# Kernel optimization log

Measured on AMD Instinct MI355X. Metric: run time of the kernel, lower is better.

Reference implementation:

```python
import jax, jax.numpy as jnp
import numpy as np

EMBED = 1024
HEADS = 16
HEAD_DIM = EMBED // HEADS


def setup_inputs() -> dict:
    key = jax.random.key(0)
    ks = jax.random.split(key, 8)
    N, L = 4, 2048
    inp = {
        "values": jax.random.normal(ks[0], (N, L, EMBED), dtype=jnp.float32),
        "keys": jax.random.normal(ks[1], (N, L, EMBED), dtype=jnp.float32),
        "query": jax.random.normal(ks[2], (N, L, EMBED), dtype=jnp.float32),
        # per-head-dim projections (torch Linear: y = x @ W.T), no bias
        "Wv": jax.random.normal(ks[3], (HEAD_DIM, HEAD_DIM), dtype=jnp.float32) * (1.0 / np.sqrt(HEAD_DIM)),
        "Wk": jax.random.normal(ks[4], (HEAD_DIM, HEAD_DIM), dtype=jnp.float32) * (1.0 / np.sqrt(HEAD_DIM)),
        "Wq": jax.random.normal(ks[5], (HEAD_DIM, HEAD_DIM), dtype=jnp.float32) * (1.0 / np.sqrt(HEAD_DIM)),
        # output projection with bias
        "Wo": jax.random.normal(ks[6], (EMBED, EMBED), dtype=jnp.float32) * (1.0 / np.sqrt(EMBED)),
        "bo": jax.random.normal(ks[7], (EMBED,), dtype=jnp.float32) * 0.01,
    }
    return inp


def reference(values, keys, query, Wv, Wk, Wq, Wo, bo):
    N, Lq, _ = query.shape
    Lv = values.shape[1]
    Lk = keys.shape[1]
    # split heads: [N, L, H, D]
    v = values.reshape(N, Lv, HEADS, HEAD_DIM)
    k = keys.reshape(N, Lk, HEADS, HEAD_DIM)
    q = query.reshape(N, Lq, HEADS, HEAD_DIM)
    # per-head-dim linear projections (x @ W.T)
    v = jnp.einsum("nlhd,ed->nlhe", v, Wv)
    k = jnp.einsum("nlhd,ed->nlhe", k, Wk)
    q = jnp.einsum("nlhd,ed->nlhe", q, Wq)
    # scores: [N, H, Q, K]; note scale is sqrt(embed_size), matching source
    energy = jnp.einsum("nqhd,nkhd->nhqk", q, k)
    attention = jax.nn.softmax(energy / jnp.sqrt(jnp.float32(EMBED)), axis=-1)
    # weighted values: [N, Q, H, D] -> [N, Q, E]
    out = jnp.einsum("nhql,nlhd->nqhd", attention, v).reshape(N, Lq, EMBED)
    # output projection
    return out @ Wo.T + bo
```

## Files before the change

### kernel.cpp

```cpp
#include <hip/hip_runtime.h>
#include <hip/hip_bf16.h>

typedef __bf16 bf16;
typedef __bf16 bf16x2 __attribute__((ext_vector_type(2)));
typedef __bf16 bf16x4 __attribute__((ext_vector_type(4)));
typedef __bf16 bf16x8 __attribute__((ext_vector_type(8)));
typedef float f32x4 __attribute__((ext_vector_type(4)));

#define MFMA16(a, b, c) __builtin_amdgcn_mfma_f32_16x16x32_bf16((a), (b), (c), 0, 0, 0)

#if __has_builtin(__builtin_amdgcn_exp2f)
#define EXP2(x) __builtin_amdgcn_exp2f(x)
#else
#define EXP2(x) exp2f(x)
#endif

constexpr int EMBED = 1024;
constexpr int HEADS = 16;
constexpr int HD = 64;
constexpr int SEQ = 2048;
constexpr int LDSP = 72;
constexpr int SXTP = 76;
constexpr int WO_N = EMBED * EMBED;

#define QSCALE 0.04508422082f

static __device__ __forceinline__ unsigned pack2(float a, float b) {
    bf16x2 t;
    t[0] = (bf16)a;
    t[1] = (bf16)b;
    return __builtin_bit_cast(unsigned, t);
}
#define SWAP32(x, y) asm("v_permlane32_swap_b32 %0, %1" : "+v"(x), "+v"(y))
#define SWAP16(x, y) asm("v_permlane16_swap_b32 %0, %1" : "+v"(x), "+v"(y))

__global__ __launch_bounds__(256) void convert_weights(
    const float* __restrict__ Wo, const float* __restrict__ Wq,
    const float* __restrict__ Wk, const float* __restrict__ Wv,
    bf16* __restrict__ Wob, bf16* __restrict__ Wqb,
    bf16* __restrict__ Wkb, bf16* __restrict__ Wvb) {
    int gid = blockIdx.x * 256 + threadIdx.x;
    int base = gid * 8;
    const float* src;
    bf16* dst;
    float sc = 1.0f;
    int off;
    if (base < WO_N) {
        src = Wo; dst = Wob; off = base;
    } else {
        int j = base - WO_N;
        int w = j >> 12;
        off = j & 4095;
        src = (w == 0) ? Wq : (w == 1) ? Wk : Wv;
        dst = (w == 0) ? Wqb : (w == 1) ? Wkb : Wvb;
        if (w == 0) sc = QSCALE;
    }
    float4 a = *(const float4*)(src + off);
    float4 b = *(const float4*)(src + off + 4);
    bf16x8 o;
    o[0] = (bf16)(a.x * sc); o[1] = (bf16)(a.y * sc);
    o[2] = (bf16)(a.z * sc); o[3] = (bf16)(a.w * sc);
    o[4] = (bf16)(b.x * sc); o[5] = (bf16)(b.y * sc);
    o[6] = (bf16)(b.z * sc); o[7] = (bf16)(b.w * sc);
    *(bf16x8*)(dst + off) = o;
}

__global__ __launch_bounds__(256) void proj_kernel(
    const float* __restrict__ Vx, const float* __restrict__ Kx, const float* __restrict__ Qx,
    const bf16* __restrict__ Wqb, const bf16* __restrict__ Wkb, const bf16* __restrict__ Wvb,
    bf16* __restrict__ Vt, bf16* __restrict__ Kp, bf16* __restrict__ Qp) {
    __shared__ __align__(16) bf16 sT[64 * LDSP];
    __shared__ __align__(16) bf16 sXT[64 * SXTP];
    int t = threadIdx.x, lane = t & 63, wq = t >> 6;
    int m = lane & 15, q8 = lane >> 4;
    int rowbase = blockIdx.x * 64;
    int Arow = rowbase + wq * 16 + m;
    const float* Xs[3] = {Qx, Kx, Vx};
    const bf16* Ws[3] = {Wqb, Wkb, Wvb};
    f32x4 z = {0.f, 0.f, 0.f, 0.f};

    for (int ts = 0; ts < 3; ts++) {
        bf16x8 af[2];
        for (int c = 0; c < 2; c++) {
            const float* s = Xs[ts] + (size_t)Arow * 64 + c * 32 + q8 * 8;
            float4 x0 = *(const float4*)s;
            float4 x1 = *(const float4*)(s + 4);
            bf16x8 a;
            a[0] = (bf16)x0.x; a[1] = (bf16)x0.y; a[2] = (bf16)x0.z; a[3] = (bf16)x0.w;
            a[4] = (bf16)x1.x; a[5] = (bf16)x1.y; a[6] = (bf16)x1.z; a[7] = (bf16)x1.w;
            af[c] = a;
        }
        bf16x8 bfr[4][2];
        for (int nt = 0; nt < 4; nt++)
            for (int c = 0; c < 2; c++)
                bfr[nt][c] = *(const bf16x8*)(Ws[ts] + (nt * 16 + m) * 64 + c * 32 + q8 * 8);
        f32x4 acc[4] = {z, z, z, z};
        for (int c = 0; c < 2; c++)
            for (int nt = 0; nt < 4; nt++)
                acc[nt] = MFMA16(af[c], bfr[nt][c], acc[nt]);

        if (ts < 2) {
            __syncthreads();
            for (int nt = 0; nt < 4; nt++)
                for (int jr = 0; jr < 4; jr++)
                    sT[(wq * 16 + q8 * 4 + jr) * LDSP + nt * 16 + m] = (bf16)acc[nt][jr];
            __syncthreads();
            int r = t >> 2, c4 = t & 3;
            int R = rowbase + r;
            int h = R & 15, l = (R >> 4) & 2047, n = R >> 15;
            bf16* dst = ((ts == 0) ? Qp : Kp) + ((size_t)(n * HEADS + h) * SEQ + l) * HD + c4 * 16;
            bf16x8 v0 = *(const bf16x8*)&sT[r * LDSP + c4 * 16];
            bf16x8 v1 = *(const bf16x8*)&sT[r * LDSP + c4 * 16 + 8];
            *(bf16x8*)dst = v0;
            *(bf16x8*)(dst + 8) = v1;
        } else {
            for (int nt = 0; nt < 4; nt++) {
                bf16x4 pv;
                pv[0] = (bf16)acc[nt][0]; pv[1] = (bf16)acc[nt][1];
                pv[2] = (bf16)acc[nt][2]; pv[3] = (bf16)acc[nt][3];
                *(bf16x4*)&sXT[(nt * 16 + m) * SXTP + wq * 16 + q8 * 4] = pv;
            }
            __syncthreads();
            int n = rowbase >> 15, l0 = (rowbase >> 4) & 2047;
            for (int i = t; i < 1024; i += 256) {
                int e = i & 63, hh = i >> 6;
                bf16x4 pv;
                pv[0] = sXT[e * SXTP + 0 * 16 + hh];
                pv[1] = sXT[e * SXTP + 1 * 16 + hh];
                pv[2] = sXT[e * SXTP + 2 * 16 + hh];
                pv[3] = sXT[e * SXTP + 3 * 16 + hh];
                *(bf16x4*)(Vt + ((size_t)(n * HEADS + hh) * HD + e) * SEQ + l0) = pv;
            }
        }
    }
}

__global__ __launch_bounds__(256, 2) void flash_kernel(
    const bf16* __restrict__ Qp, const bf16* __restrict__ Kp, const bf16* __restrict__ Vt,
    bf16* __restrict__ O) {
    int nh = blockIdx.x, qt = blockIdx.y;
    int n = nh >> 4, h = nh & 15;
    int t = threadIdx.x, lane = t & 63, wq = t >> 6;
    int m = lane & 15, q8 = lane >> 4;
    __shared__ __align__(16) bf16 sK[64 * LDSP];
    __shared__ __align__(16) bf16 sV[64 * LDSP];
    size_t nhs = (size_t)nh;
    int qb = qt * 256 + wq * 64;
    const bf16* Qb = Qp + (nhs * SEQ + qb) * HD;
    const bf16* Kb = Kp + nhs * SEQ * HD;
    const bf16* Vb = Vt + nhs * (size_t)HD * SEQ;

    bool isK = t < 128;
    int t2 = isK ? t : t - 128;
    int srow = t2 >> 1, shalf = t2 & 1;
    const bf16* sbase = isK ? (Kb + (size_t)srow * HD + shalf * 32)
                            : (Vb + (size_t)srow * SEQ + shalf * 32);
    size_t sstride = isK ? (size_t)HD : 1;
    bf16* ldst = (isK ? sK : sV) + srow * LDSP + shalf * 32;

    bf16x8 qf[4][2];
    for (int ntq = 0; ntq < 4; ntq++)
        for (int c = 0; c < 2; c++)
            qf[ntq][c] = *(const bf16x8*)(Qb + (ntq * 16 + m) * HD + c * 32 + q8 * 8);

    bf16x8 ones;
    for (int i = 0; i < 8; i++) ones[i] = (bf16)1.0f;

    f32x4 z = {0.f, 0.f, 0.f, 0.f};
    f32x4 accO[4][4];
    for (int a = 0; a < 4; a++)
        for (int b = 0; b < 4; b++) accO[a][b] = z;
    f32x4 accL[4] = {z, z, z, z};

    bf16x8 stg[4];
    auto load_stage = [&](int kb) {
#pragma unroll
        for (int j = 0; j < 4; j++)
            stg[j] = *(const bf16x8*)(sbase + (size_t)kb * sstride + j * 8);
    };
    auto write_stage = [&]() {
#pragma unroll
        for (int j = 0; j < 4; j++)
            *(bf16x8*)(ldst + j * 8) = stg[j];
    };

    load_stage(0);
    write_stage();
    __syncthreads();
    load_stage(64);

    for (int kb = 0; kb < SEQ; kb += 64) {
        bf16x8 kf[4][2];
#pragma unroll
        for (int kt = 0; kt < 4; kt++)
#pragma unroll
            for (int c = 0; c < 2; c++)
                kf[kt][c] = *(const bf16x8*)&sK[(kt * 16 + m) * LDSP + c * 32 + q8 * 8];
        bf16x8 vf[4][2];
#pragma unroll
        for (int dt = 0; dt < 4; dt++)
#pragma unroll
            for (int c = 0; c < 2; c++)
                vf[dt][c] = *(const bf16x8*)&sV[(dt * 16 + m) * LDSP + c * 32 + q8 * 8];
        __syncthreads();
        write_stage();
        __syncthreads();
        load_stage((kb + 128) & (SEQ - 1));

#pragma unroll
        for (int ntq = 0; ntq < 4; ntq++) {
            f32x4 st[4];
#pragma unroll
            for (int kt = 0; kt < 4; kt++) st[kt] = z;
#pragma unroll
            for (int c = 0; c < 2; c++)
#pragma unroll
                for (int kt = 0; kt < 4; kt++)
                    st[kt] = MFMA16(kf[kt][c], qf[ntq][c], st[kt]);
            f32x4 pr[4];
#pragma unroll
            for (int kt = 0; kt < 4; kt++) {
                pr[kt][0] = EXP2(st[kt][0]);
                pr[kt][1] = EXP2(st[kt][1]);
                pr[kt][2] = EXP2(st[kt][2]);
                pr[kt][3] = EXP2(st[kt][3]);
            }
            bf16x8 pf[2];
#pragma unroll
            for (int c = 0; c < 2; c++) {
                unsigned dw[4];
#pragma unroll
                for (int i = 0; i < 2; i++) {
                    unsigned u = pack2(pr[2 * c][2 * i], pr[2 * c][2 * i + 1]);
                    unsigned v = pack2(pr[2 * c + 1][2 * i], pr[2 * c + 1][2 * i + 1]);
                    SWAP32(u, v);
                    SWAP16(u, v);
                    dw[i] = u;
                    dw[2 + i] = v;
                }
                union { unsigned u[4]; bf16x8 v; } cvt;
                cvt.u[0] = dw[0]; cvt.u[1] = dw[1];
                cvt.u[2] = dw[2]; cvt.u[3] = dw[3];
                pf[c] = cvt.v;
            }
#pragma unroll
            for (int c = 0; c < 2; c++) {
#pragma unroll
                for (int dt = 0; dt < 4; dt++)
                    accO[ntq][dt] = MFMA16(pf[c], vf[dt][c], accO[ntq][dt]);
                accL[ntq] = MFMA16(pf[c], ones, accL[ntq]);
            }
        }
    }

    for (int mtq = 0; mtq < 4; mtq++)
        for (int j = 0; j < 4; j++) {
            float iv = 1.0f / accL[mtq][j];
            int q = qb + mtq * 16 + q8 * 4 + j;
            size_t ro = ((size_t)n * SEQ + q) * EMBED + h * HD;
            for (int dt = 0; dt < 4; dt++)
                O[ro + dt * 16 + m] = (bf16)(accO[mtq][dt][j] * iv);
        }
}

__global__ __launch_bounds__(256) void outproj_kernel(
    const bf16* __restrict__ O, const bf16* __restrict__ Wob,
    const float* __restrict__ bo, float* __restrict__ out) {
    int et = blockIdx.x, qt = blockIdx.y;
    int t = threadIdx.x, lane = t & 63, wq = t >> 6;
    int m = lane & 15, q8 = lane >> 4;
    int qb = qt * 128 + wq * 32;
    const bf16* Ob = O + (size_t)qb * EMBED;
    const bf16* Wb = Wob + (size_t)et * 64 * EMBED;
    f32x4 z = {0.f, 0.f, 0.f, 0.f};
    f32x4 acc[2][4];
    for (int a = 0; a < 2; a++)
        for (int b = 0; b < 4; b++) acc[a][b] = z;

    bf16x8 afA[2], bfA[4], afB[2], bfB[4];
    auto loadA = [&](int kk) {
        for (int mt = 0; mt < 2; mt++)
            afA[mt] = *(const bf16x8*)(Ob + (size_t)(mt * 16 + m) * EMBED + kk + q8 * 8);
        for (int nt = 0; nt < 4; nt++)
            bfA[nt] = *(const bf16x8*)(Wb + (size_t)(nt * 16 + m) * EMBED + kk + q8 * 8);
    };
    auto loadB = [&](int kk) {
        for (int mt = 0; mt < 2; mt++)
            afB[mt] = *(const bf16x8*)(Ob + (size_t)(mt * 16 + m) * EMBED + kk + q8 * 8);
        for (int nt = 0; nt < 4; nt++)
            bfB[nt] = *(const bf16x8*)(Wb + (size_t)(nt * 16 + m) * EMBED + kk + q8 * 8);
    };
    loadA(0);
    loadB(32);
    for (int kk = 0; kk < EMBED; kk += 64) {
        for (int mt = 0; mt < 2; mt++)
            for (int nt = 0; nt < 4; nt++)
                acc[mt][nt] = MFMA16(afA[mt], bfA[nt], acc[mt][nt]);
        loadA((kk + 64) & (EMBED - 1));
        for (int mt = 0; mt < 2; mt++)
            for (int nt = 0; nt < 4; nt++)
                acc[mt][nt] = MFMA16(afB[mt], bfB[nt], acc[mt][nt]);
        loadB((kk + 96) & (EMBED - 1));
    }
    for (int nt = 0; nt < 4; nt++) {
        int col = et * 64 + nt * 16 + m;
        float bias = bo[col];
        for (int mt = 0; mt < 2; mt++)
            for (int j = 0; j < 4; j++) {
                int q = qb + mt * 16 + q8 * 4 + j;
                out[(size_t)q * EMBED + col] = acc[mt][nt][j] + bias;
            }
    }
}

extern "C" void kernel_launch(void* const* d_in, const int* in_sizes, int n_in,
                              void* d_out, int out_size, void* d_ws, size_t ws_size,
                              hipStream_t stream) {
    const float* values = (const float*)d_in[0];
    const float* keys   = (const float*)d_in[1];
    const float* query  = (const float*)d_in[2];
    const float* Wv     = (const float*)d_in[3];
    const float* Wk     = (const float*)d_in[4];
    const float* Wq     = (const float*)d_in[5];
    const float* Wo     = (const float*)d_in[6];
    const float* bo     = (const float*)d_in[7];
    float* out = (float*)d_out;

    char* ws = (char*)d_ws;
    bf16* Qp  = (bf16*)(ws);
    bf16* Kp  = (bf16*)(ws + (size_t)(16 << 20));
    bf16* Vt  = (bf16*)(ws + (size_t)(32 << 20));
    bf16* O   = (bf16*)(ws + (size_t)(48 << 20));
    bf16* Wob = (bf16*)(ws + (size_t)(64 << 20));
    bf16* Wqb = (bf16*)(ws + (size_t)(66 << 20));
    bf16* Wkb = (bf16*)(ws + (size_t)(66 << 20) + 8192);
    bf16* Wvb = (bf16*)(ws + (size_t)(66 << 20) + 16384);

    hipLaunchKernelGGL(convert_weights, dim3(518), dim3(256), 0, stream,
                       Wo, Wq, Wk, Wv, Wob, Wqb, Wkb, Wvb);
    hipLaunchKernelGGL(proj_kernel, dim3(2048), dim3(256), 0, stream,
                       values, keys, query, Wqb, Wkb, Wvb, Vt, Kp, Qp);
    hipLaunchKernelGGL(flash_kernel, dim3(64, 8), dim3(256), 0, stream, Qp, Kp, Vt, O);
    hipLaunchKernelGGL(outproj_kernel, dim3(16, 64), dim3(256), 0, stream, O, Wob, bo, out);
}
```

Measured before the change: 334.7 us.

## Tile output projection GEMM through LDS with 128x128 blocks and XCD-aware mapping

Rewrites the output projection so each block stages 128x128 tiles of O and Wo in LDS with register-prefetched double buffering. Each wave then computes a 64x64 sub-tile, replacing the old scheme where every wave read its operands directly from global memory. The grid becomes 1D with an XCD-aware remap so neighbouring query tiles share an L2, and launch bounds now request 2 blocks per CU. The intent is to cut redundant global traffic and raise MFMA reuse per load, at the cost of more LDS, extra barriers and higher register pressure.

```diff
diff --git a/kernel.cpp b/kernel.cpp
--- a/kernel.cpp
+++ b/kernel.cpp
@@ -263,51 +263,79 @@
         }
 }
 
-__global__ __launch_bounds__(256) void outproj_kernel(
+__global__ __launch_bounds__(256, 2) void outproj_kernel(
     const bf16* __restrict__ O, const bf16* __restrict__ Wob,
     const float* __restrict__ bo, float* __restrict__ out) {
-    int et = blockIdx.x, qt = blockIdx.y;
+    __shared__ __align__(16) bf16 sA[128 * LDSP];
+    __shared__ __align__(16) bf16 sB[128 * LDSP];
+    int bid = blockIdx.x;
+    int xcd = bid & 7, idx = bid >> 3;
+    int qt = xcd * 8 + (idx & 7), et = idx >> 3;
     int t = threadIdx.x, lane = t & 63, wq = t >> 6;
     int m = lane & 15, q8 = lane >> 4;
-    int qb = qt * 128 + wq * 32;
-    const bf16* Ob = O + (size_t)qb * EMBED;
-    const bf16* Wb = Wob + (size_t)et * 64 * EMBED;
+    int wr = wq >> 1, wc = wq & 1;
+    int qb = qt * 128, cb = et * 128;
+
+    bool isA = t < 128;
+    int r = t & 127;
+    const bf16* sbase = isA ? (O + (size_t)(qb + r) * EMBED)
+                            : (Wob + (size_t)(cb + r) * EMBED);
+    bf16* ldst = (isA ? sA : sB) + r * LDSP;
+
+    bf16x8 stg[8];
+    auto load_stage = [&](int kk) {
+#pragma unroll
+        for (int j = 0; j < 8; j++)
+            stg[j] = *(const bf16x8*)(sbase + kk + j * 8);
+    };
+    auto write_stage = [&]() {
+#pragma unroll
+        for (int j = 0; j < 8; j++)
+            *(bf16x8*)(ldst + j * 8) = stg[j];
+    };
+
     f32x4 z = {0.f, 0.f, 0.f, 0.f};
-    f32x4 acc[2][4];
-    for (int a = 0; a < 2; a++)
+    f32x4 acc[4][4];
+    for (int a = 0; a < 4; a++)
         for (int b = 0; b < 4; b++) acc[a][b] = z;
 
-    bf16x8 afA[2], bfA[4], afB[2], bfB[4];
-    auto loadA = [&](int kk) {
-        for (int mt = 0; mt < 2; mt++)
-            afA[mt] = *(const bf16x8*)(Ob + (size_t)(mt * 16 + m) * EMBED + kk + q8 * 8);
+    load_stage(0);
+    write_stage();
+    __syncthreads();
+    load_stage(64);
+
+    for (int kk = 0; kk < EMBED; kk += 64) {
+        bf16x8 af[4][2], bfr[4][2];
+#pragma unroll
+        for (int mt = 0; mt < 4; mt++)
+#pragma unroll
+            for (int c = 0; c < 2; c++)
+                af[mt][c] = *(const bf16x8*)&sA[(wr * 64 + mt * 16 + m) * LDSP + c * 32 + q8 * 8];
+#pragma unroll
         for (int nt = 0; nt < 4; nt++)
-            bfA[nt] = *(const bf16x8*)(Wb + (size_t)(nt * 16 + m) * EMBED + kk + q8 * 8);
-    };
-    auto loadB = [&](int kk) {
-        for (int mt = 0; mt < 2; mt++)
-            afB[mt] = *(const bf16x8*)(Ob + (size_t)(mt * 16 + m) * EMBED + kk + q8 * 8);
-        for (int nt = 0; nt < 4; nt++)
-            bfB[nt] = *(const bf16x8*)(Wb + (size_t)(nt * 16 + m) * EMBED + kk + q8 * 8);
-    };
-    loadA(0);
-    loadB(32);
-    for (int kk = 0; kk < EMBED; kk += 64) {
-        for (int mt = 0; mt < 2; mt++)
-            for (int nt = 0; nt < 4; nt++)
-                acc[mt][nt] = MFMA16(afA[mt], bfA[nt], acc[mt][nt]);
-        loadA((kk + 64) & (EMBED - 1));
-        for (int mt = 0; mt < 2; mt++)
-            for (int nt = 0; nt < 4; nt++)
-                acc[mt][nt] = MFMA16(afB[mt], bfB[nt], acc[mt][nt]);
-        loadB((kk + 96) & (EMBED - 1));
-    }
+#pragma unroll
+            for (int c = 0; c < 2; c++)
+                bfr[nt][c] = *(const bf16x8*)&sB[(wc * 64 + nt * 16 + m) * LDSP + c * 32 + q8 * 8];
+        __syncthreads();
+        write_stage();
+        __syncthreads();
+        load_stage((kk + 128) & (EMBED - 1));
+
+#pragma unroll
+        for (int c = 0; c < 2; c++)
+#pragma unroll
+            for (int mt = 0; mt < 4; mt++)
+#pragma unroll
+                for (int nt = 0; nt < 4; nt++)
+                    acc[mt][nt] = MFMA16(af[mt][c], bfr[nt][c], acc[mt][nt]);
+    }
+
     for (int nt = 0; nt < 4; nt++) {
-        int col = et * 64 + nt * 16 + m;
+        int col = cb + wc * 64 + nt * 16 + m;
         float bias = bo[col];
-        for (int mt = 0; mt < 2; mt++)
+        for (int mt = 0; mt < 4; mt++)
             for (int j = 0; j < 4; j++) {
-                int q = qb + mt * 16 + q8 * 4 + j;
+                int q = qb + wr * 64 + mt * 16 + q8 * 4 + j;
                 out[(size_t)q * EMBED + col] = acc[mt][nt][j] + bias;
             }
     }
@@ -341,5 +369,5 @@
     hipLaunchKernelGGL(proj_kernel, dim3(2048), dim3(256), 0, stream,
                        values, keys, query, Wqb, Wkb, Wvb, Vt, Kp, Qp);
     hipLaunchKernelGGL(flash_kernel, dim3(64, 8), dim3(256), 0, stream, Qp, Kp, Vt, O);
-    hipLaunchKernelGGL(outproj_kernel, dim3(16, 64), dim3(256), 0, stream, O, Wob, bo, out);
-}
+    hipLaunchKernelGGL(outproj_kernel, dim3(512), dim3(256), 0, stream, O, Wob, bo, out);
+}
```

Measured after the change: 280.7 us. -16.1%, faster.
